# Performance work log

Measured on AMD Instinct MI355X. Metric: run time of the kernel, lower is better.

Reference implementation:

```python
import jax, jax.numpy as jnp
import numpy as np

B, S, M = 8, 2048, 256
D = 512          # input/memory feature dim
P = 512          # proj_dim
H = 8            # num_heads


def setup_inputs() -> dict:
    key = jax.random.key(0)
    ks = jax.random.split(key, 10)
    sc = 0.02
    return {
        "input_seq": jax.random.normal(ks[0], (B, S, D), jnp.float32),
        "memory_cells": jax.random.normal(ks[1], (B, M, D), jnp.float32),
        "Wk": jax.random.normal(ks[2], (D, P), jnp.float32) * sc,
        "bk": jnp.zeros((P,), jnp.float32),
        "Wv": jax.random.normal(ks[3], (D, P), jnp.float32) * sc,
        "bv": jnp.zeros((P,), jnp.float32),
        "Wq": jax.random.normal(ks[4], (H, D, P), jnp.float32) * sc,  # stacked per-head query Dense
        "bq": jnp.zeros((H, P), jnp.float32),
        "Wo": jax.random.normal(ks[5], (H * P, P), jnp.float32) * sc,
        "bo": jnp.zeros((P,), jnp.float32),
    }


def reference(input_seq, memory_cells, Wk, bk, Wv, bv, Wq, bq, Wo, bo):
    # shared key/value projections (multi-query: one K/V for all heads)
    ik = input_seq @ Wk + bk          # [B,S,P]
    mk = memory_cells @ Wk + bk       # [B,M,P]
    iv = input_seq @ Wv + bv          # [B,S,P]
    mv = memory_cells @ Wv + bv       # [B,M,P]

    # per-head queries from memory cells, all heads at once
    q = jnp.einsum('bmd,hdp->bhmp', memory_cells, Wq) + bq[None, :, None, :]  # [B,H,M,P]

    input_score = jnp.einsum('bhmp,bsp->bhms', q, ik)          # [B,H,M,S]
    self_score = jnp.sum(q * mk[:, None], axis=-1, keepdims=True)  # [B,H,M,1]
    score = jnp.concatenate([self_score, input_score], axis=-1)    # [B,H,M,S+1]
    score = score / jnp.sqrt(jnp.float32(P))
    attn = jax.nn.softmax(score, axis=-1)

    self_attn = attn[..., 0:1]                                  # [B,H,M,1]
    input_attn = attn[..., 1:]                                  # [B,H,M,S]
    val = jnp.einsum('bhms,bsp->bhmp', input_attn, iv) + self_attn * mv[:, None]

    # concat heads: [B,M,H*P]
    concat = jnp.transpose(val, (0, 2, 1, 3)).reshape(B, M, H * P)
    return concat @ Wo + bo           # [B,M,P]
```

## Files before the change

kernel.cpp:

```cpp
#include <hip/hip_runtime.h>

#define B_ 8
#define S_ 2048
#define M_ 256
#define D_ 512
#define P_ 512
#define H_ 8

#define SCALE 0.044194173824159216f

typedef __attribute__((ext_vector_type(8))) short bf16x8;
typedef __attribute__((ext_vector_type(4))) float f32x4;

static __device__ __forceinline__ float bf2f(short u) {
  union { float f; unsigned int i; } x;
  x.i = ((unsigned int)(unsigned short)u) << 16;
  return x.f;
}
static __device__ __forceinline__ short f2bf(float f) {
  union { float f; unsigned int i; } x;
  x.f = f;
  unsigned int r = (x.i + 0x7FFFu + ((x.i >> 16) & 1u)) >> 16;
  return (short)r;
}

static __device__ __forceinline__ void gll16(const short* g, short* l) {
  __builtin_amdgcn_global_load_lds(
      (const __attribute__((address_space(1))) void*)g,
      (__attribute__((address_space(3))) void*)l, 16, 0, 0);
}

#define LGKM_WAIT() asm volatile("s_waitcnt lgkmcnt(0)" ::: "memory")
#define VM_WAIT0() asm volatile("s_waitcnt vmcnt(0)" ::: "memory")
#define SCHED_FENCE() asm volatile("" ::: "memory")

__global__ __launch_bounds__(256) void cast_both(
    const float* __restrict__ inA, short* __restrict__ outA, int n4A,
    const float* __restrict__ inM, short* __restrict__ outM)
{
  int idx = blockIdx.x * 256 + threadIdx.x;
  const float* in = inA;
  short* out = outA;
  if (idx >= n4A) { idx -= n4A; in = inM; out = outM; }
  float4 v = ((const float4*)in)[idx];
  short o0 = f2bf(v.x), o1 = f2bf(v.y), o2 = f2bf(v.z), o3 = f2bf(v.w);
  uint2 pk;
  pk.x = (unsigned int)(unsigned short)o0 | ((unsigned int)(unsigned short)o1 << 16);
  pk.y = (unsigned int)(unsigned short)o2 | ((unsigned int)(unsigned short)o3 << 16);
  ((uint2*)out)[idx] = pk;
}

__global__ __launch_bounds__(256) void wtrans_g(
    const float* __restrict__ in, short* __restrict__ out, int kdim, int ndim)
{
  __shared__ float tile[32][33];
  const int t = threadIdx.x, tx = t & 31, ty = t >> 5;
  const size_t zofs = (size_t)blockIdx.z * kdim * ndim;
  const int n0 = blockIdx.x * 32, k0 = blockIdx.y * 32;
  const float* inp = in + zofs;
  short* outp = out + zofs;
#pragma unroll
  for (int i = 0; i < 4; ++i)
    tile[ty + 8 * i][tx] = inp[(size_t)(k0 + ty + 8 * i) * ndim + n0 + tx];
  __syncthreads();
#pragma unroll
  for (int i = 0; i < 4; ++i)
    outp[(size_t)(n0 + ty + 8 * i) * kdim + k0 + tx] = f2bf(tile[tx][ty + 8 * i]);
}

__global__ __launch_bounds__(256) void zero_f(float* __restrict__ p) {
  ((float4*)p)[blockIdx.x * 256 + threadIdx.x] = make_float4(0.f, 0.f, 0.f, 0.f);
}

template<int MODE, int K, int N, int LDA, int LDB>
__global__ __launch_bounds__(256) void gemm128(
    const short* __restrict__ Abase, const short* __restrict__ Bbase,
    const float* __restrict__ bias, void* __restrict__ Cv,
    const size_t aZ, const int bzsh, const size_t bZ, const size_t cZ,
    float* __restrict__ Ls,
    const float* __restrict__ eselfp, const short* __restrict__ mvbp)
{
  __shared__ short As[8192];
  __shared__ short Bs[8192];
  const int t = threadIdx.x;
  const int w = t >> 6, lane = t & 63, qd = lane >> 4, ln = lane & 15;
  const int z = blockIdx.z;
  const int n0 = blockIdx.x * 128, m0 = blockIdx.y * 128;
  const int wm = (w & 1) * 64, wn = (w >> 1) * 64;

  const short* A  = Abase + (size_t)z * aZ;
  const short* Bp = Bbase + (size_t)(z >> bzsh) * bZ;

  const int rr = t >> 2, g0 = t & 3;
  const int gs0 = g0 ^ ((rr >> 1) & 3);
  const int gs1 = g0 ^ (((rr + 64) >> 1) & 3);
  const short* ga0 = A + (size_t)(m0 + rr) * LDA + gs0 * 8;
  const short* ga1 = A + (size_t)(m0 + rr + 64) * LDA + gs1 * 8;
  const short* gb0 = Bp + (size_t)(n0 + rr) * LDB + gs0 * 8;
  const short* gb1 = Bp + (size_t)(n0 + rr + 64) * LDB + gs1 * 8;

  int aoff[4], boff[4];
#pragma unroll
  for (int mt = 0; mt < 4; ++mt) {
    int r = wm + mt * 16 + ln;
    aoff[mt] = r * 32 + (qd ^ ((r >> 1) & 3)) * 8;
  }
#pragma unroll
  for (int nt = 0; nt < 4; ++nt) {
    int r = wn + nt * 16 + ln;
    boff[nt] = r * 32 + (qd ^ ((r >> 1) & 3)) * 8;
  }

  f32x4 acc[4][4];
#pragma unroll
  for (int mt = 0; mt < 4; ++mt)
#pragma unroll
    for (int nt = 0; nt < 4; ++nt) acc[mt][nt] = (f32x4){0.f, 0.f, 0.f, 0.f};

  constexpr int NIT = K / 32;
  gll16(ga0, &As[w * 512]);
  gll16(ga1, &As[2048 + w * 512]);
  gll16(gb0, &Bs[w * 512]);
  gll16(gb1, &Bs[2048 + w * 512]);

  for (int k = 0; k < NIT; ++k) {
    VM_WAIT0();
    __syncthreads();
    const int cb = (k & 1) * 4096;
    bf16x8 af[4], bfr[4];
#pragma unroll
    for (int mt = 0; mt < 4; ++mt) af[mt] = *(const bf16x8*)&As[cb + aoff[mt]];
#pragma unroll
    for (int nt = 0; nt < 4; ++nt) bfr[nt] = *(const bf16x8*)&Bs[cb + boff[nt]];
    SCHED_FENCE();
    if (k + 1 < NIT) {
      const int kc = (k + 1) * 32;
      const int nb = ((k + 1) & 1) * 4096;
      gll16(ga0 + kc, &As[nb + w * 512]);
      gll16(ga1 + kc, &As[nb + 2048 + w * 512]);
      gll16(gb0 + kc, &Bs[nb + w * 512]);
      gll16(gb1 + kc, &Bs[nb + 2048 + w * 512]);
    }
#pragma unroll
    for (int mt = 0; mt < 4; ++mt)
#pragma unroll
      for (int nt = 0; nt < 4; ++nt)
        acc[mt][nt] = __builtin_amdgcn_mfma_f32_16x16x32_bf16(af[mt], bfr[nt], acc[mt][nt], 0, 0, 0);
  }

  if constexpr (MODE == 5) {
#pragma unroll
    for (int nt = 0; nt < 4; ++nt) {
      const int col = n0 + wn + nt * 16 + ln;
#pragma unroll
      for (int mt = 0; mt < 4; ++mt)
#pragma unroll
        for (int r = 0; r < 4; ++r) {
          const int row = m0 + wm + mt * 16 + qd * 4 + r;
          ((float*)Cv)[(size_t)z * cZ + (size_t)row * N + col] = acc[mt][nt][r];
        }
    }
  } else if constexpr (MODE == 2) {
#pragma unroll
    for (int mt = 0; mt < 4; ++mt)
#pragma unroll
      for (int nt = 0; nt < 4; ++nt)
#pragma unroll
        for (int r = 0; r < 4; ++r)
          acc[mt][nt][r] = __expf(acc[mt][nt][r] * SCALE);
#pragma unroll
    for (int mt = 0; mt < 4; ++mt)
#pragma unroll
      for (int r = 0; r < 4; ++r) {
        float rsum = acc[mt][0][r] + acc[mt][1][r] + acc[mt][2][r] + acc[mt][3][r];
        rsum += __shfl_xor(rsum, 1);
        rsum += __shfl_xor(rsum, 2);
        rsum += __shfl_xor(rsum, 4);
        rsum += __shfl_xor(rsum, 8);
        if (ln == 0) {
          const int row = m0 + wm + mt * 16 + qd * 4 + r;
          atomicAdd(&Ls[(size_t)z * M_ + row], rsum);
        }
      }
#pragma unroll
    for (int nt = 0; nt < 4; ++nt) {
      const int col = n0 + wn + nt * 16 + ln;
#pragma unroll
      for (int mt = 0; mt < 4; ++mt)
#pragma unroll
        for (int r = 0; r < 4; ++r) {
          const int row = m0 + wm + mt * 16 + qd * 4 + r;
          ((short*)Cv)[(size_t)z * cZ + (size_t)row * N + col] = f2bf(acc[mt][nt][r]);
        }
    }
  } else if constexpr (MODE == 3) {
    const int zb = z >> 3, hh = z & 7;
#pragma unroll
    for (int mt = 0; mt < 4; ++mt)
#pragma unroll
      for (int r = 0; r < 4; ++r) {
        const int row = m0 + wm + mt * 16 + qd * 4 + r;
        const float es = eselfp[(size_t)z * M_ + row];
        const float inv = 1.f / (es + Ls[(size_t)z * M_ + row]);
        const short* mvr = mvbp + ((size_t)(zb * M_ + row)) * P_;
        short* outr = (short*)Cv + ((size_t)(zb * M_ + row)) * (H_ * P_) + (size_t)hh * P_;
#pragma unroll
        for (int nt = 0; nt < 4; ++nt) {
          const int col = n0 + wn + nt * 16 + ln;
          outr[col] = f2bf((acc[mt][nt][r] + es * bf2f(mvr[col])) * inv);
        }
      }
  } else {
#pragma unroll
    for (int nt = 0; nt < 4; ++nt) {
      const int col = n0 + wn + nt * 16 + ln;
      const float bc = bias[512 * z + col];
#pragma unroll
      for (int mt = 0; mt < 4; ++mt)
#pragma unroll
        for (int r = 0; r < 4; ++r) {
          const int row = m0 + wm + mt * 16 + qd * 4 + r;
          const int bidx = row >> 8, ml = row & 255;
          ((short*)Cv)[((size_t)(bidx * H_ + z) * M_ + ml) * N + col] = f2bf(acc[mt][nt][r] + bc);
        }
    }
  }
}

template<bool TRANSV>
__global__ __launch_bounds__(256) void proj_kv(
    const short* __restrict__ A,
    const short* __restrict__ WkT, const short* __restrict__ WvT,
    const float* __restrict__ bk, const float* __restrict__ bv,
    short* __restrict__ Ck, short* __restrict__ Cvv)
{
  __shared__ short As[8192];
  __shared__ short Bks[4096];
  __shared__ short Bvs[4096];
  const int t = threadIdx.x;
  const int w = t >> 6, lane = t & 63, qd = lane >> 4, ln = lane & 15;
  const int n0 = blockIdx.x * 64, m0 = blockIdx.y * 128;
  const int wm = (w & 1) * 64, wn2 = (w >> 1) * 32;

  const int rr = t >> 2, g0 = t & 3;
  const int gs0 = g0 ^ ((rr >> 1) & 3);
  const int gs1 = g0 ^ (((rr + 64) >> 1) & 3);
  const short* ga0 = A + (size_t)(m0 + rr) * 512 + gs0 * 8;
  const short* ga1 = A + (size_t)(m0 + rr + 64) * 512 + gs1 * 8;
  const short* gbk = WkT + (size_t)(n0 + rr) * 512 + gs0 * 8;
  const short* gbv = WvT + (size_t)(n0 + rr) * 512 + gs0 * 8;

  int aoff[4], boff[2];
#pragma unroll
  for (int mt = 0; mt < 4; ++mt) {
    int r = wm + mt * 16 + ln;
    aoff[mt] = r * 32 + (qd ^ ((r >> 1) & 3)) * 8;
  }
#pragma unroll
  for (int nt = 0; nt < 2; ++nt) {
    int r = wn2 + nt * 16 + ln;
    boff[nt] = r * 32 + (qd ^ ((r >> 1) & 3)) * 8;
  }

  f32x4 accK[4][2], accV[4][2];
#pragma unroll
  for (int mt = 0; mt < 4; ++mt)
#pragma unroll
    for (int nt = 0; nt < 2; ++nt) {
      accK[mt][nt] = (f32x4){0.f, 0.f, 0.f, 0.f};
      accV[mt][nt] = (f32x4){0.f, 0.f, 0.f, 0.f};
    }

  gll16(ga0, &As[w * 512]);
  gll16(ga1, &As[2048 + w * 512]);
  gll16(gbk, &Bks[w * 512]);
  gll16(gbv, &Bvs[w * 512]);

  for (int k = 0; k < 16; ++k) {
    VM_WAIT0();
    __syncthreads();
    const int ca = (k & 1) * 4096, cbk = (k & 1) * 2048;
    bf16x8 af[4], bkf[2], bvf[2];
#pragma unroll
    for (int mt = 0; mt < 4; ++mt) af[mt] = *(const bf16x8*)&As[ca + aoff[mt]];
#pragma unroll
    for (int nt = 0; nt < 2; ++nt) {
      bkf[nt] = *(const bf16x8*)&Bks[cbk + boff[nt]];
      bvf[nt] = *(const bf16x8*)&Bvs[cbk + boff[nt]];
    }
    SCHED_FENCE();
    if (k + 1 < 16) {
      const int kc = (k + 1) * 32;
      const int na = ((k + 1) & 1) * 4096, nb = ((k + 1) & 1) * 2048;
      gll16(ga0 + kc, &As[na + w * 512]);
      gll16(ga1 + kc, &As[na + 2048 + w * 512]);
      gll16(gbk + kc, &Bks[nb + w * 512]);
      gll16(gbv + kc, &Bvs[nb + w * 512]);
    }
#pragma unroll
    for (int mt = 0; mt < 4; ++mt)
#pragma unroll
      for (int nt = 0; nt < 2; ++nt) {
        accK[mt][nt] = __builtin_amdgcn_mfma_f32_16x16x32_bf16(af[mt], bkf[nt], accK[mt][nt], 0, 0, 0);
        accV[mt][nt] = __builtin_amdgcn_mfma_f32_16x16x32_bf16(af[mt], bvf[nt], accV[mt][nt], 0, 0, 0);
      }
  }

#pragma unroll
  for (int nt = 0; nt < 2; ++nt) {
    const int col = n0 + wn2 + nt * 16 + ln;
    const float bc = bk[col];
#pragma unroll
    for (int mt = 0; mt < 4; ++mt)
#pragma unroll
      for (int r = 0; r < 4; ++r) {
        const int row = m0 + wm + mt * 16 + qd * 4 + r;
        Ck[(size_t)row * 512 + col] = f2bf(accK[mt][nt][r] + bc);
      }
  }

  if constexpr (!TRANSV) {
#pragma unroll
    for (int nt = 0; nt < 2; ++nt) {
      const int col = n0 + wn2 + nt * 16 + ln;
      const float bc = bv[col];
#pragma unroll
      for (int mt = 0; mt < 4; ++mt)
#pragma unroll
        for (int r = 0; r < 4; ++r) {
          const int row = m0 + wm + mt * 16 + qd * 4 + r;
          Cvv[(size_t)row * 512 + col] = f2bf(accV[mt][nt][r] + bc);
        }
    }
  } else {
    __syncthreads();
    short* ep = &As[w * 1280];
    const int lr = lane >> 1, lc16 = (lane & 1) * 16;
#pragma unroll
    for (int pass = 0; pass < 2; ++pass) {
#pragma unroll
      for (int mh = 0; mh < 2; ++mh) {
        const int mt = pass * 2 + mh;
#pragma unroll
        for (int nt = 0; nt < 2; ++nt) {
          const float bc = bv[n0 + wn2 + nt * 16 + ln];
#pragma unroll
          for (int r = 0; r < 4; ++r)
            ep[(nt * 16 + ln) * 40 + mh * 16 + qd * 4 + r] = f2bf(accV[mt][nt][r] + bc);
        }
      }
      LGKM_WAIT();
      const int srow0 = m0 + wm + pass * 32;
      const int bidx = srow0 >> 11;
      const int sloc = (srow0 & 2047) + lc16;
      const int pcol = n0 + wn2 + lr;
      short* outp = Cvv + (size_t)bidx * P_ * S_ + (size_t)pcol * S_ + sloc;
      *(bf16x8*)outp = *(const bf16x8*)&ep[lr * 40 + lc16];
      *(bf16x8*)(outp + 8) = *(const bf16x8*)&ep[lr * 40 + lc16 + 8];
      LGKM_WAIT();
    }
  }
}

__global__ __launch_bounds__(256) void reduce_wo(
    const float* __restrict__ partial, const float* __restrict__ bo,
    float* __restrict__ out)
{
  const int idx4 = blockIdx.x * 256 + threadIdx.x;
  float4 s = ((const float4*)bo)[idx4 & 127];
#pragma unroll
  for (int zz = 0; zz < 4; ++zz) {
    float4 p = ((const float4*)partial)[(size_t)zz * 262144 + idx4];
    s.x += p.x; s.y += p.y; s.z += p.z; s.w += p.w;
  }
  ((float4*)out)[idx4] = s;
}

__global__ __launch_bounds__(256) void selfscore(
    const short* __restrict__ qb, const short* __restrict__ mkb,
    float* __restrict__ eself)
{
  const int z = blockIdx.x, t = threadIdx.x;
  const short* qr = qb + ((size_t)z * M_ + t) * P_;
  const short* mr = mkb + ((size_t)(z >> 3) * M_ + t) * P_;
  float s = 0.f;
#pragma unroll 8
  for (int c = 0; c < P_; c += 8) {
    bf16x8 qv = *(const bf16x8*)(qr + c);
    bf16x8 mv = *(const bf16x8*)(mr + c);
#pragma unroll
    for (int j = 0; j < 8; ++j) s += bf2f(qv[j]) * bf2f(mv[j]);
  }
  eself[(size_t)z * M_ + t] = __expf(s * SCALE);
}

extern "C" void kernel_launch(void* const* d_in, const int* in_sizes, int n_in,
                              void* d_out, int out_size, void* d_ws, size_t ws_size,
                              hipStream_t stream) {
  const float* input_seq = (const float*)d_in[0];
  const float* memcells  = (const float*)d_in[1];
  const float* Wk = (const float*)d_in[2];
  const float* bk = (const float*)d_in[3];
  const float* Wv = (const float*)d_in[4];
  const float* bv = (const float*)d_in[5];
  const float* Wq = (const float*)d_in[6];
  const float* bq = (const float*)d_in[7];
  const float* Wo = (const float*)d_in[8];
  const float* bo = (const float*)d_in[9];
  float* out = (float*)d_out;

  short* ws = (short*)d_ws;
  size_t o = 0;
  short* valb = ws + o; o += (size_t)B_ * M_ * H_ * P_;
  short* WoT  = ws + o; o += (size_t)(H_ * P_) * P_;
  short* mvb  = ws + o; o += (size_t)B_ * M_ * P_;
  short* mkb  = ws + o; o += (size_t)B_ * M_ * P_;
  short* qb   = ws + o; o += (size_t)B_ * H_ * M_ * P_;
  short* ivT  = ws + o; o += (size_t)B_ * P_ * S_;
  short* ikb  = ws + o; o += (size_t)B_ * S_ * P_;
  float* partial = (float*)(ws + o); o += (size_t)B_ * H_ * M_ * P_;
  float* eself = (float*)(ws + o); o += 2 * (size_t)B_ * H_ * M_;
  float* Ls    = (float*)(ws + o); o += 2 * (size_t)B_ * H_ * M_;
  short* region2 = ws + o;
  short* Ab  = region2;
  short* Mb  = Ab + (size_t)B_ * S_ * D_;
  short* WkT = Mb + (size_t)B_ * M_ * D_;
  short* WvT = WkT + (size_t)D_ * P_;
  short* WqT = WvT + (size_t)D_ * P_;
  short* Eb  = region2;

  dim3 blk(256);

  const int n4A = B_ * S_ * D_ / 4;
  const int n4M = B_ * M_ * D_ / 4;
  cast_both<<<dim3((n4A + n4M) / 256), blk, 0, stream>>>(input_seq, Ab, n4A, memcells, Mb);
  wtrans_g<<<dim3(16, 16, 1), blk, 0, stream>>>(Wk, WkT, 512, 512);
  wtrans_g<<<dim3(16, 16, 1), blk, 0, stream>>>(Wv, WvT, 512, 512);
  wtrans_g<<<dim3(16, 16, 8), blk, 0, stream>>>(Wq, WqT, 512, 512);
  wtrans_g<<<dim3(16, 128, 1), blk, 0, stream>>>(Wo, WoT, 4096, 512);

  proj_kv<true><<<dim3(8, 128), blk, 0, stream>>>(Ab, WkT, WvT, bk, bv, ikb, ivT);
  proj_kv<false><<<dim3(8, 16), blk, 0, stream>>>(Mb, WkT, WvT, bk, bv, mkb, mvb);

  gemm128<1, 512, 512, 512, 512><<<dim3(4, 16, 8), blk, 0, stream>>>(
      Mb, WqT, bq, qb, 0, 0, (size_t)D_ * P_, 0, nullptr, nullptr, nullptr);

  zero_f<<<dim3(16), blk, 0, stream>>>(Ls);
  gemm128<2, 512, 2048, 512, 512><<<dim3(16, 2, 64), blk, 0, stream>>>(
      qb, ikb, nullptr, Eb, (size_t)M_ * P_, 3, (size_t)S_ * P_,
      (size_t)M_ * S_, Ls, nullptr, nullptr);

  selfscore<<<dim3(64), blk, 0, stream>>>(qb, mkb, eself);

  gemm128<3, 2048, 512, 2048, 2048><<<dim3(4, 2, 64), blk, 0, stream>>>(
      Eb, ivT, nullptr, valb, (size_t)M_ * S_, 3, (size_t)P_ * S_,
      0, Ls, eself, mvb);

  gemm128<5, 1024, 512, 4096, 4096><<<dim3(4, 16, 4), blk, 0, stream>>>(
      valb, WoT, nullptr, partial, 1024, 0, 1024,
      (size_t)2048 * 512, nullptr, nullptr, nullptr);
  reduce_wo<<<dim3(1024), blk, 0, stream>>>(partial, bo, out);
}
```

Before: 335.6 us.

## Single-buffer GEMM LDS, remap attention grids by batch, fuse weight transposes and zeroing

The GEMM and K/V projection kernels drop double-buffered LDS prefetching in favour of a single buffer with load, barrier, compute, which halves shared memory per block so more blocks can be resident. The attention GEMMs get a new grid mapping with batch in blockIdx.x and head/m-block in z, which changes the order in which blocks that share the same K/V operand are scheduled. The weight transposes for Wk, Wv and Wq are merged into one launch, and zeroing of Ls moves into the selfscore kernel, removing two launches. The cost is that global loads no longer overlap with MFMA compute inside a block, which may slow the main loop.

```diff
diff --git a/kernel.cpp b/kernel.cpp
--- a/kernel.cpp
+++ b/kernel.cpp
@@ -31,8 +31,6 @@
 }
 
 #define LGKM_WAIT() asm volatile("s_waitcnt lgkmcnt(0)" ::: "memory")
-#define VM_WAIT0() asm volatile("s_waitcnt vmcnt(0)" ::: "memory")
-#define SCHED_FENCE() asm volatile("" ::: "memory")
 
 __global__ __launch_bounds__(256) void cast_both(
     const float* __restrict__ inA, short* __restrict__ outA, int n4A,
@@ -50,46 +48,76 @@
   ((uint2*)out)[idx] = pk;
 }
 
-__global__ __launch_bounds__(256) void wtrans_g(
-    const float* __restrict__ in, short* __restrict__ out, int kdim, int ndim)
+__global__ __launch_bounds__(256) void wtrans_all(
+    const float* __restrict__ Wk, const float* __restrict__ Wv,
+    const float* __restrict__ Wq,
+    short* __restrict__ WkT, short* __restrict__ WvT, short* __restrict__ WqT)
 {
   __shared__ float tile[32][33];
   const int t = threadIdx.x, tx = t & 31, ty = t >> 5;
-  const size_t zofs = (size_t)blockIdx.z * kdim * ndim;
+  const int z = blockIdx.z;
+  const float* inp;
+  short* outp;
+  if (z == 0)      { inp = Wk; outp = WkT; }
+  else if (z == 1) { inp = Wv; outp = WvT; }
+  else             { inp = Wq + (size_t)(z - 2) * 512 * 512;
+                     outp = WqT + (size_t)(z - 2) * 512 * 512; }
   const int n0 = blockIdx.x * 32, k0 = blockIdx.y * 32;
-  const float* inp = in + zofs;
-  short* outp = out + zofs;
 #pragma unroll
   for (int i = 0; i < 4; ++i)
-    tile[ty + 8 * i][tx] = inp[(size_t)(k0 + ty + 8 * i) * ndim + n0 + tx];
+    tile[ty + 8 * i][tx] = inp[(size_t)(k0 + ty + 8 * i) * 512 + n0 + tx];
   __syncthreads();
 #pragma unroll
   for (int i = 0; i < 4; ++i)
-    outp[(size_t)(n0 + ty + 8 * i) * kdim + k0 + tx] = f2bf(tile[tx][ty + 8 * i]);
-}
-
-__global__ __launch_bounds__(256) void zero_f(float* __restrict__ p) {
-  ((float4*)p)[blockIdx.x * 256 + threadIdx.x] = make_float4(0.f, 0.f, 0.f, 0.f);
+    outp[(size_t)(n0 + ty + 8 * i) * 512 + k0 + tx] = f2bf(tile[tx][ty + 8 * i]);
+}
+
+__global__ __launch_bounds__(256) void wtrans_wo(
+    const float* __restrict__ in, short* __restrict__ out)
+{
+  __shared__ float tile[32][33];
+  const int t = threadIdx.x, tx = t & 31, ty = t >> 5;
+  const int n0 = blockIdx.x * 32, k0 = blockIdx.y * 32;
+#pragma unroll
+  for (int i = 0; i < 4; ++i)
+    tile[ty + 8 * i][tx] = in[(size_t)(k0 + ty + 8 * i) * 512 + n0 + tx];
+  __syncthreads();
+#pragma unroll
+  for (int i = 0; i < 4; ++i)
+    out[(size_t)(n0 + ty + 8 * i) * 4096 + k0 + tx] = f2bf(tile[tx][ty + 8 * i]);
 }
 
 template<int MODE, int K, int N, int LDA, int LDB>
 __global__ __launch_bounds__(256) void gemm128(
     const short* __restrict__ Abase, const short* __restrict__ Bbase,
     const float* __restrict__ bias, void* __restrict__ Cv,
-    const size_t aZ, const int bzsh, const size_t bZ, const size_t cZ,
+    const size_t aZ, const size_t bZ, const size_t cZ,
     float* __restrict__ Ls,
     const float* __restrict__ eselfp, const short* __restrict__ mvbp)
 {
-  __shared__ short As[8192];
-  __shared__ short Bs[8192];
+  __shared__ short As[4096];
+  __shared__ short Bs[4096];
   const int t = threadIdx.x;
   const int w = t >> 6, lane = t & 63, qd = lane >> 4, ln = lane & 15;
-  const int z = blockIdx.z;
-  const int n0 = blockIdx.x * 128, m0 = blockIdx.y * 128;
   const int wm = (w & 1) * 64, wn = (w >> 1) * 64;
 
+  int z, m0, n0, bsel;
+  if constexpr (MODE == 2 || MODE == 3) {
+    const int b = blockIdx.x;
+    n0 = blockIdx.y * 128;
+    const int h = blockIdx.z & 7, mb = blockIdx.z >> 3;
+    z = b * 8 + h;
+    m0 = mb * 128;
+    bsel = b;
+  } else {
+    n0 = blockIdx.x * 128;
+    m0 = blockIdx.y * 128;
+    z = blockIdx.z;
+    bsel = z;
+  }
+
   const short* A  = Abase + (size_t)z * aZ;
-  const short* Bp = Bbase + (size_t)(z >> bzsh) * bZ;
+  const short* Bp = Bbase + (size_t)bsel * bZ;
 
   const int rr = t >> 2, g0 = t & 3;
   const int gs0 = g0 ^ ((rr >> 1) & 3);
@@ -117,30 +145,19 @@
 #pragma unroll
     for (int nt = 0; nt < 4; ++nt) acc[mt][nt] = (f32x4){0.f, 0.f, 0.f, 0.f};
 
-  constexpr int NIT = K / 32;
-  gll16(ga0, &As[w * 512]);
-  gll16(ga1, &As[2048 + w * 512]);
-  gll16(gb0, &Bs[w * 512]);
-  gll16(gb1, &Bs[2048 + w * 512]);
-
-  for (int k = 0; k < NIT; ++k) {
-    VM_WAIT0();
+  for (int kc = 0; kc < K; kc += 32) {
     __syncthreads();
-    const int cb = (k & 1) * 4096;
+    gll16(ga0 + kc, &As[w * 512]);
+    gll16(ga1 + kc, &As[2048 + w * 512]);
+    gll16(gb0 + kc, &Bs[w * 512]);
+    gll16(gb1 + kc, &Bs[2048 + w * 512]);
+    __syncthreads();
+
     bf16x8 af[4], bfr[4];
 #pragma unroll
-    for (int mt = 0; mt < 4; ++mt) af[mt] = *(const bf16x8*)&As[cb + aoff[mt]];
-#pragma unroll
-    for (int nt = 0; nt < 4; ++nt) bfr[nt] = *(const bf16x8*)&Bs[cb + boff[nt]];
-    SCHED_FENCE();
-    if (k + 1 < NIT) {
-      const int kc = (k + 1) * 32;
-      const int nb = ((k + 1) & 1) * 4096;
-      gll16(ga0 + kc, &As[nb + w * 512]);
-      gll16(ga1 + kc, &As[nb + 2048 + w * 512]);
-      gll16(gb0 + kc, &Bs[nb + w * 512]);
-      gll16(gb1 + kc, &Bs[nb + 2048 + w * 512]);
-    }
+    for (int mt = 0; mt < 4; ++mt) af[mt] = *(const bf16x8*)&As[aoff[mt]];
+#pragma unroll
+    for (int nt = 0; nt < 4; ++nt) bfr[nt] = *(const bf16x8*)&Bs[boff[nt]];
 #pragma unroll
     for (int mt = 0; mt < 4; ++mt)
 #pragma unroll
@@ -234,9 +251,10 @@
     const float* __restrict__ bk, const float* __restrict__ bv,
     short* __restrict__ Ck, short* __restrict__ Cvv)
 {
-  __shared__ short As[8192];
-  __shared__ short Bks[4096];
-  __shared__ short Bvs[4096];
+  __shared__ short Sh[8192];
+  short* As  = Sh;
+  short* Bks = Sh + 4096;
+  short* Bvs = Sh + 6144;
   const int t = threadIdx.x;
   const int w = t >> 6, lane = t & 63, qd = lane >> 4, ln = lane & 15;
   const int n0 = blockIdx.x * 64, m0 = blockIdx.y * 128;
@@ -271,31 +289,21 @@
       accV[mt][nt] = (f32x4){0.f, 0.f, 0.f, 0.f};
     }
 
-  gll16(ga0, &As[w * 512]);
-  gll16(ga1, &As[2048 + w * 512]);
-  gll16(gbk, &Bks[w * 512]);
-  gll16(gbv, &Bvs[w * 512]);
-
-  for (int k = 0; k < 16; ++k) {
-    VM_WAIT0();
+  for (int kc = 0; kc < 512; kc += 32) {
     __syncthreads();
-    const int ca = (k & 1) * 4096, cbk = (k & 1) * 2048;
+    gll16(ga0 + kc, &As[w * 512]);
+    gll16(ga1 + kc, &As[2048 + w * 512]);
+    gll16(gbk + kc, &Bks[w * 512]);
+    gll16(gbv + kc, &Bvs[w * 512]);
+    __syncthreads();
+
     bf16x8 af[4], bkf[2], bvf[2];
 #pragma unroll
-    for (int mt = 0; mt < 4; ++mt) af[mt] = *(const bf16x8*)&As[ca + aoff[mt]];
+    for (int mt = 0; mt < 4; ++mt) af[mt] = *(const bf16x8*)&As[aoff[mt]];
 #pragma unroll
     for (int nt = 0; nt < 2; ++nt) {
-      bkf[nt] = *(const bf16x8*)&Bks[cbk + boff[nt]];
-      bvf[nt] = *(const bf16x8*)&Bvs[cbk + boff[nt]];
-    }
-    SCHED_FENCE();
-    if (k + 1 < 16) {
-      const int kc = (k + 1) * 32;
-      const int na = ((k + 1) & 1) * 4096, nb = ((k + 1) & 1) * 2048;
-      gll16(ga0 + kc, &As[na + w * 512]);
-      gll16(ga1 + kc, &As[na + 2048 + w * 512]);
-      gll16(gbk + kc, &Bks[nb + w * 512]);
-      gll16(gbv + kc, &Bvs[nb + w * 512]);
+      bkf[nt] = *(const bf16x8*)&Bks[boff[nt]];
+      bvf[nt] = *(const bf16x8*)&Bvs[boff[nt]];
     }
 #pragma unroll
     for (int mt = 0; mt < 4; ++mt)
@@ -334,7 +342,7 @@
     }
   } else {
     __syncthreads();
-    short* ep = &As[w * 1280];
+    short* ep = &Sh[w * 1280];
     const int lr = lane >> 1, lc16 = (lane & 1) * 16;
 #pragma unroll
     for (int pass = 0; pass < 2; ++pass) {
@@ -378,7 +386,7 @@
 
 __global__ __launch_bounds__(256) void selfscore(
     const short* __restrict__ qb, const short* __restrict__ mkb,
-    float* __restrict__ eself)
+    float* __restrict__ eself, float* __restrict__ Ls)
 {
   const int z = blockIdx.x, t = threadIdx.x;
   const short* qr = qb + ((size_t)z * M_ + t) * P_;
@@ -392,6 +400,7 @@
     for (int j = 0; j < 8; ++j) s += bf2f(qv[j]) * bf2f(mv[j]);
   }
   eself[(size_t)z * M_ + t] = __expf(s * SCALE);
+  Ls[(size_t)z * M_ + t] = 0.f;
 }
 
 extern "C" void kernel_launch(void* const* d_in, const int* in_sizes, int n_in,
@@ -434,30 +443,27 @@
   const int n4A = B_ * S_ * D_ / 4;
   const int n4M = B_ * M_ * D_ / 4;
   cast_both<<<dim3((n4A + n4M) / 256), blk, 0, stream>>>(input_seq, Ab, n4A, memcells, Mb);
-  wtrans_g<<<dim3(16, 16, 1), blk, 0, stream>>>(Wk, WkT, 512, 512);
-  wtrans_g<<<dim3(16, 16, 1), blk, 0, stream>>>(Wv, WvT, 512, 512);
-  wtrans_g<<<dim3(16, 16, 8), blk, 0, stream>>>(Wq, WqT, 512, 512);
-  wtrans_g<<<dim3(16, 128, 1), blk, 0, stream>>>(Wo, WoT, 4096, 512);
+  wtrans_all<<<dim3(16, 16, 10), blk, 0, stream>>>(Wk, Wv, Wq, WkT, WvT, WqT);
+  wtrans_wo<<<dim3(16, 128), blk, 0, stream>>>(Wo, WoT);
 
   proj_kv<true><<<dim3(8, 128), blk, 0, stream>>>(Ab, WkT, WvT, bk, bv, ikb, ivT);
   proj_kv<false><<<dim3(8, 16), blk, 0, stream>>>(Mb, WkT, WvT, bk, bv, mkb, mvb);
 
   gemm128<1, 512, 512, 512, 512><<<dim3(4, 16, 8), blk, 0, stream>>>(
-      Mb, WqT, bq, qb, 0, 0, (size_t)D_ * P_, 0, nullptr, nullptr, nullptr);
-
-  zero_f<<<dim3(16), blk, 0, stream>>>(Ls);
-  gemm128<2, 512, 2048, 512, 512><<<dim3(16, 2, 64), blk, 0, stream>>>(
-      qb, ikb, nullptr, Eb, (size_t)M_ * P_, 3, (size_t)S_ * P_,
+      Mb, WqT, bq, qb, 0, (size_t)D_ * P_, 0, nullptr, nullptr, nullptr);
+
+  selfscore<<<dim3(64), blk, 0, stream>>>(qb, mkb, eself, Ls);
+
+  gemm128<2, 512, 2048, 512, 512><<<dim3(8, 16, 16), blk, 0, stream>>>(
+      qb, ikb, nullptr, Eb, (size_t)M_ * P_, (size_t)S_ * P_,
       (size_t)M_ * S_, Ls, nullptr, nullptr);
 
-  selfscore<<<dim3(64), blk, 0, stream>>>(qb, mkb, eself);
-
-  gemm128<3, 2048, 512, 2048, 2048><<<dim3(4, 2, 64), blk, 0, stream>>>(
-      Eb, ivT, nullptr, valb, (size_t)M_ * S_, 3, (size_t)P_ * S_,
+  gemm128<3, 2048, 512, 2048, 2048><<<dim3(8, 4, 16), blk, 0, stream>>>(
+      Eb, ivT, nullptr, valb, (size_t)M_ * S_, (size_t)P_ * S_,
       0, Ls, eself, mvb);
 
   gemm128<5, 1024, 512, 4096, 4096><<<dim3(4, 16, 4), blk, 0, stream>>>(
-      valb, WoT, nullptr, partial, 1024, 0, 1024,
+      valb + 0, WoT, nullptr, partial, 1024, 1024,
       (size_t)2048 * 512, nullptr, nullptr, nullptr);
   reduce_wo<<<dim3(1024), blk, 0, stream>>>(partial, bo, out);
 }
```

Result: no change. 336.2 us (+0.2%).
